# Kernel optimization log

Measured on AMD Instinct MI355X. Metric: run time of the kernel, lower is better.

The kernel has to match this reference:

```python
import jax, jax.numpy as jnp
import numpy as np

B = 4096      # batch
F = 16        # num fields
V = 20000     # field vocab size
E = 64        # embed size
HID = 1024    # hidden width (all hidden layers equal, required by the reshape trick)
NODE_IN = F * E  # 1024
NL = 3        # number of hidden layers stacked into attention (len(layer_sizes)-2)


def _xavier(key, shape):
    fan_in, fan_out = shape[0], shape[1]
    lim = np.sqrt(6.0 / (fan_in + fan_out)).astype(np.float32)
    return jax.random.uniform(key, shape, jnp.float32, -lim, lim)


def setup_inputs() -> dict:
    key = jax.random.key(0)
    ks = jax.random.split(key, 8)
    idx = jax.random.randint(ks[0], (B, F), 0, V)
    emb = _xavier(ks[1], (V, E))  # share init shape, then tile per-field via fold_in
    emb = jnp.stack([_xavier(jax.random.fold_in(ks[1], f), (V, E)) for f in range(F)], axis=0)  # [F,V,E]
    w0 = _xavier(ks[2], (NODE_IN, HID)); b0 = jnp.zeros((HID,), jnp.float32)
    w1 = _xavier(ks[3], (HID, HID));     b1 = jnp.zeros((HID,), jnp.float32)
    w2 = _xavier(ks[4], (HID, HID));     b2 = jnp.zeros((HID,), jnp.float32)
    w3 = _xavier(ks[5], (HID, HID));     b3 = jnp.zeros((HID,), jnp.float32)
    w_final = _xavier(ks[6], (2 * HID, 1)); b_final = jnp.zeros((1,), jnp.float32)
    return {"idx": idx, "emb": emb, "w0": w0, "b0": b0, "w1": w1, "b1": b1,
            "w2": w2, "b2": b2, "w3": w3, "b3": b3,
            "w_final": w_final, "b_final": b_final}


def reference(idx, emb, w0, b0, w1, b1, w2, b2, w3, b3, w_final, b_final):
    bsz = idx.shape[0]
    # sparse one-hot @ embed == gather: [B,F,E] -> [B, F*E]
    xw = emb[jnp.arange(F)[None, :], idx].reshape(bsz, F * E)
    # MLP stack (dropout in test mode: keep_prob=1, i.e. identity)
    l0 = jax.nn.relu(xw @ w0 + b0)
    l1 = jax.nn.relu(l0 @ w1 + b1)
    l2 = jax.nn.relu(l1 @ w2 + b2)
    l_final = jax.nn.relu(l2 @ w3 + b3)
    # faithful reproduction of tf.concat(axis=0) then reshape([-1, NL, HID])
    cat = jnp.concatenate([l0, l1, l2], axis=0)          # [NL*B, HID]
    Hm = cat.reshape(bsz, NL, HID)                        # H[b,j] = cat[NL*b + j]
    mask = 1.0 - jnp.eye(NL, dtype=Hm.dtype)              # zero diagonal
    S = jnp.einsum('bih,bjh->bij', Hm, Hm) * mask         # [B, NL, NL]
    A = jax.nn.softmax(S, axis=-1)                        # attention over layers
    G = jnp.einsum('bij,bjh->bh', A, Hm)                  # reduce_sum(A@H, axis=1)
    M = jnp.concatenate([l_final, G], axis=1)             # [B, 2*HID]
    out = (M @ w_final + b_final).squeeze(-1)             # logits [B]
    return out
```

## Files before the change

### kernel.cpp

```cpp
#include <hip/hip_runtime.h>
#include <hip/hip_bf16.h>
#include <stdint.h>

#define B_SZ 4096
#define F_N 16
#define V_SZ 20000
#define E_SZ 64
#define HID 1024

typedef __attribute__((ext_vector_type(8))) _Float16 f16x8;
typedef __attribute__((ext_vector_type(4))) _Float16 f16x4;
typedef __attribute__((ext_vector_type(4))) float f32x4;

__device__ __forceinline__ void gload16(const void* g, void* l) {
  __builtin_amdgcn_global_load_lds(
      (const __attribute__((address_space(1))) void*)g,
      (__attribute__((address_space(3))) void*)l, 16, 0, 0);
}

__device__ __forceinline__ int s3(int r) { return (r ^ (r >> 3)) & 7; }

__global__ __launch_bounds__(256) void prep(
    const int* __restrict__ idx, const float* __restrict__ emb,
    const float* __restrict__ w0, _Float16* __restrict__ wt0,
    _Float16* __restrict__ xw) {
  const int cb = blockIdx.x;
  const int t = threadIdx.x;
  if (cb < 512) {
    __shared__ float tile[64][33];
    const int k0 = (cb >> 5) * 64, n0 = (cb & 31) * 32;
    const int c = t & 31;
#pragma unroll
    for (int q = 0; q < 8; ++q) {
      int r = (t >> 5) + q * 8;
      tile[r][c] = w0[(size_t)(k0 + r) * HID + n0 + c];
    }
    __syncthreads();
#pragma unroll
    for (int q = 0; q < 4; ++q) {
      int s = t + q * 256;
      int n = s >> 5, c2 = s & 31;
      union { _Float16 h[2]; uint32_t u; } p;
      p.h[0] = (_Float16)tile[2 * c2][n];
      p.h[1] = (_Float16)tile[2 * c2 + 1][n];
      *(uint32_t*)(wt0 + (size_t)(n0 + n) * HID + k0 + 2 * c2) = p.u;
    }
  } else {
    int i = (cb - 512) * 256 + t;
    int b = i >> 8;
    int r = i & 255;
    int f = r >> 4;
    int e4 = r & 15;
    int id = idx[b * F_N + f];
    float4 v = *(const float4*)(emb + ((size_t)f * V_SZ + id) * E_SZ + e4 * 4);
    f16x4 h = {(_Float16)v.x, (_Float16)v.y, (_Float16)v.z, (_Float16)v.w};
    *(f16x4*)(xw + (size_t)b * HID + r * 4) = h;
  }
}

__global__ __launch_bounds__(512) void gemm_mfma(
    const _Float16* __restrict__ A, const _Float16* __restrict__ Wt,
    const float* __restrict__ bias, _Float16* __restrict__ C,
    const float* __restrict__ wnx, _Float16* __restrict__ wtnx) {
  __shared__ __align__(16) char shraw[65536];
  const int t = threadIdx.x;

  if (blockIdx.x >= 256) {
    const int cv = blockIdx.x - 256;
    float (*tile)[65] = (float(*)[65])shraw;
    const int k0 = (cv >> 4) * 64, n0 = (cv & 15) * 64;
    const int c = t & 63;
#pragma unroll
    for (int q = 0; q < 8; ++q) {
      int r = (t >> 6) + q * 8;
      tile[r][c] = wnx[(size_t)(k0 + r) * HID + n0 + c];
    }
    __syncthreads();
    {
      int n = t >> 3, ch = t & 7;
      f16x8 v;
#pragma unroll
      for (int j = 0; j < 8; ++j) v[j] = (_Float16)tile[ch * 8 + j][n];
      *(f16x8*)(wtnx + (size_t)(n0 + n) * HID + k0 + ch * 8) = v;
    }
    return;
  }

#define AS(b) ((_Float16*)(shraw + (b) * 32768))
#define BS(b) ((_Float16*)(shraw + (b) * 32768 + 16384))

  const int l = ((blockIdx.x & 7) << 5) | (blockIdx.x >> 3);
  const int bm = (l >> 3) * 128, bn = (l & 7) * 128;

  const int w = t >> 6, lane = t & 63;
  const int wk = w & 1, wn = (w >> 1) & 1, wm = w >> 2;
  const int lr = lane & 15, lg = lane >> 4;

  const int srow = t >> 3, cdst = t & 7;
  const int csrc = cdst ^ s3(srow);
  const _Float16* ga0 = A + (size_t)(bm + srow) * HID + csrc * 8;
  const _Float16* gb0 = Wt + (size_t)(bn + srow) * HID + csrc * 8;
  const int ld0 = t * 8, ld1 = t * 8 + 4096;

  int aoff[4], boff[4];
#pragma unroll
  for (int i = 0; i < 4; i++) {
    int ra = wm * 64 + i * 16 + lr;
    aoff[i] = ra * 64 + (((wk * 4 + lg) ^ s3(ra)) * 8);
    int rb = wn * 64 + i * 16 + lr;
    boff[i] = rb * 64 + (((wk * 4 + lg) ^ s3(rb)) * 8);
  }

  f32x4 acc[4][4] = {};

#define STAGE(buf, ko)                                   \
  gload16(ga0 + (ko), &AS(buf)[ld0]);                    \
  gload16(ga0 + (ko) + (size_t)64 * HID, &AS(buf)[ld1]); \
  gload16(gb0 + (ko), &BS(buf)[ld0]);                    \
  gload16(gb0 + (ko) + (size_t)64 * HID, &BS(buf)[ld1]);

  STAGE(0, 0)

  for (int tI = 0; tI < 16; ++tI) {
    const int cur = tI & 1;
    if (tI < 15) {
      STAGE(cur ^ 1, (tI + 1) * 64)
    }
    if (tI < 15)
      asm volatile("s_waitcnt vmcnt(4)" ::: "memory");
    else
      asm volatile("s_waitcnt vmcnt(0)" ::: "memory");
    asm volatile("s_barrier" ::: "memory");

    f16x8 a[4], b[4];
#pragma unroll
    for (int mi = 0; mi < 4; mi++) a[mi] = *(const f16x8*)&AS(cur)[aoff[mi]];
#pragma unroll
    for (int ni = 0; ni < 4; ni++) b[ni] = *(const f16x8*)&BS(cur)[boff[ni]];
#pragma unroll
    for (int mi = 0; mi < 4; mi++)
#pragma unroll
      for (int ni = 0; ni < 4; ni++)
        acc[mi][ni] = __builtin_amdgcn_mfma_f32_16x16x32_f16(
            b[ni], a[mi], acc[mi][ni], 0, 0, 0);

    asm volatile("s_barrier" ::: "memory");
  }
#undef STAGE

  float* red = (float*)shraw;
  float* R = red + ((wm << 1) | wn) * 4096;
  if (wk == 1) {
#pragma unroll
    for (int mi = 0; mi < 4; mi++)
#pragma unroll
      for (int ni = 0; ni < 4; ni++) {
        int u = mi * 16 + lr;
        int vb = ni * 4 + lg;
        *(f32x4*)&R[u * 64 + ((vb ^ lr) << 2)] = acc[mi][ni];
      }
  }
  asm volatile("s_barrier" ::: "memory");
  if (wk == 0) {
#pragma unroll
    for (int mi = 0; mi < 4; mi++)
#pragma unroll
      for (int ni = 0; ni < 4; ni++) {
        int u = mi * 16 + lr;
        int vb = ni * 4 + lg;
        f32x4 p = *(const f32x4*)&R[u * 64 + ((vb ^ lr) << 2)];
        acc[mi][ni] += p;
      }
#pragma unroll
    for (int ni = 0; ni < 4; ni++) {
      int colb = bn + wn * 64 + ni * 16 + lg * 4;
      float4 bv = *(const float4*)&bias[colb];
#pragma unroll
      for (int mi = 0; mi < 4; mi++) {
        int row = bm + wm * 64 + mi * 16 + lr;
        f16x4 hv;
        float x0 = acc[mi][ni][0] + bv.x;
        float x1 = acc[mi][ni][1] + bv.y;
        float x2 = acc[mi][ni][2] + bv.z;
        float x3 = acc[mi][ni][3] + bv.w;
        hv[0] = (_Float16)(x0 > 0.f ? x0 : 0.f);
        hv[1] = (_Float16)(x1 > 0.f ? x1 : 0.f);
        hv[2] = (_Float16)(x2 > 0.f ? x2 : 0.f);
        hv[3] = (_Float16)(x3 > 0.f ? x3 : 0.f);
        *(f16x4*)&C[(size_t)row * HID + colb] = hv;
      }
    }
  }
#undef AS
#undef BS
}

__global__ __launch_bounds__(256) void attn_final(
    const _Float16* __restrict__ cat, const _Float16* __restrict__ lf,
    const float* __restrict__ wf, const float* __restrict__ bfin,
    float* __restrict__ out) {
  const int wave = threadIdx.x >> 6;
  const int lane = threadIdx.x & 63;
  const int b = blockIdx.x * 4 + wave;

  const _Float16* h0 = cat + (size_t)(3 * b + 0) * 1024;
  const _Float16* h1 = cat + (size_t)(3 * b + 1) * 1024;
  const _Float16* h2 = cat + (size_t)(3 * b + 2) * 1024;
  const _Float16* lfr = lf + (size_t)b * 1024;

  float s01 = 0.f, s02 = 0.f, s12 = 0.f;
  float d0 = 0.f, d1 = 0.f, d2 = 0.f, dl = 0.f;

#pragma unroll
  for (int q = 0; q < 2; ++q) {
    int e8 = (lane + q * 64) * 8;
    f16x8 a0 = *(const f16x8*)(h0 + e8);
    f16x8 a1 = *(const f16x8*)(h1 + e8);
    f16x8 a2 = *(const f16x8*)(h2 + e8);
    f16x8 al = *(const f16x8*)(lfr + e8);
    float4 u0a = *(const float4*)(wf + e8);
    float4 u0b = *(const float4*)(wf + e8 + 4);
    float4 u1a = *(const float4*)(wf + 1024 + e8);
    float4 u1b = *(const float4*)(wf + 1024 + e8 + 4);
    float wf0[8] = {u0a.x, u0a.y, u0a.z, u0a.w, u0b.x, u0b.y, u0b.z, u0b.w};
    float wf1[8] = {u1a.x, u1a.y, u1a.z, u1a.w, u1b.x, u1b.y, u1b.z, u1b.w};
#pragma unroll
    for (int j = 0; j < 8; ++j) {
      float p0 = (float)a0[j], p1 = (float)a1[j], p2 = (float)a2[j];
      float pl = (float)al[j];
      s01 = fmaf(p0, p1, s01);
      s02 = fmaf(p0, p2, s02);
      s12 = fmaf(p1, p2, s12);
      d0 = fmaf(p0, wf1[j], d0);
      d1 = fmaf(p1, wf1[j], d1);
      d2 = fmaf(p2, wf1[j], d2);
      dl = fmaf(pl, wf0[j], dl);
    }
  }

#pragma unroll
  for (int m = 1; m < 64; m <<= 1) {
    s01 += __shfl_xor(s01, m);
    s02 += __shfl_xor(s02, m);
    s12 += __shfl_xor(s12, m);
    d0 += __shfl_xor(d0, m);
    d1 += __shfl_xor(d1, m);
    d2 += __shfl_xor(d2, m);
    dl += __shfl_xor(dl, m);
  }

  if (lane == 0) {
    float c0 = 0.f, c1 = 0.f, c2 = 0.f;
    {
      float m = fmaxf(0.f, fmaxf(s01, s02));
      float e0 = expf(0.f - m), e1 = expf(s01 - m), e2 = expf(s02 - m);
      float inv = 1.f / (e0 + e1 + e2);
      c0 += e0 * inv; c1 += e1 * inv; c2 += e2 * inv;
    }
    {
      float m = fmaxf(s01, fmaxf(0.f, s12));
      float e0 = expf(s01 - m), e1 = expf(0.f - m), e2 = expf(s12 - m);
      float inv = 1.f / (e0 + e1 + e2);
      c0 += e0 * inv; c1 += e1 * inv; c2 += e2 * inv;
    }
    {
      float m = fmaxf(s02, fmaxf(s12, 0.f));
      float e0 = expf(s02 - m), e1 = expf(s12 - m), e2 = expf(0.f - m);
      float inv = 1.f / (e0 + e1 + e2);
      c0 += e0 * inv; c1 += e1 * inv; c2 += e2 * inv;
    }
    out[b] = dl + c0 * d0 + c1 * d1 + c2 * d2 + bfin[0];
  }
}

extern "C" void kernel_launch(void* const* d_in, const int* in_sizes, int n_in,
                              void* d_out, int out_size, void* d_ws,
                              size_t ws_size, hipStream_t stream) {
  const int* idx = (const int*)d_in[0];
  const float* emb = (const float*)d_in[1];
  const float* w0 = (const float*)d_in[2];
  const float* b0 = (const float*)d_in[3];
  const float* w1 = (const float*)d_in[4];
  const float* b1 = (const float*)d_in[5];
  const float* w2 = (const float*)d_in[6];
  const float* b2 = (const float*)d_in[7];
  const float* w3 = (const float*)d_in[8];
  const float* b3 = (const float*)d_in[9];
  const float* wf = (const float*)d_in[10];
  const float* bfin = (const float*)d_in[11];
  float* out = (float*)d_out;

  const size_t RB = (size_t)B_SZ * HID;
  const size_t WSZ = (size_t)HID * HID;

  _Float16* wt = (_Float16*)d_ws;
  _Float16* xw16 = wt + 4 * WSZ;
  _Float16* cat16 = xw16 + RB;
  _Float16* lf16 = cat16 + 3 * RB;

  prep<<<4608, 256, 0, stream>>>(idx, emb, w0, wt, xw16);

  gemm_mfma<<<512, 512, 0, stream>>>(xw16, wt + 0 * WSZ, b0, cat16,
                                     w1, wt + 1 * WSZ);
  gemm_mfma<<<512, 512, 0, stream>>>(cat16, wt + 1 * WSZ, b1, cat16 + RB,
                                     w2, wt + 2 * WSZ);
  gemm_mfma<<<512, 512, 0, stream>>>(cat16 + RB, wt + 2 * WSZ, b2,
                                     cat16 + 2 * RB, w3, wt + 3 * WSZ);
  gemm_mfma<<<256, 512, 0, stream>>>(cat16 + 2 * RB, wt + 3 * WSZ, b3, lf16,
                                     (const float*)nullptr,
                                     (_Float16*)nullptr);

  attn_final<<<B_SZ / 4, 256, 0, stream>>>(cat16, lf16, wf, bfin, out);
}
```

Baseline: 76.73 us.

## Fuse four MLP GEMMs into one persistent kernel with per-panel flags

Moves all four weight transposes into the prep kernel and replaces the four separate GEMM launches with a single persistent 256-block kernel. Each block loops over the layers and waits on an atomic counter for its 128-row panel of the previous layer before starting the next. This removes the launch gaps and the full-grid drain between layers, letting layers overlap across panels. The risks are spin-wait stalls and a deadlock if all 256 blocks cannot be resident at once.

```diff
diff --git a/kernel.cpp b/kernel.cpp
--- a/kernel.cpp
+++ b/kernel.cpp
@@ -22,18 +22,23 @@
 
 __global__ __launch_bounds__(256) void prep(
     const int* __restrict__ idx, const float* __restrict__ emb,
-    const float* __restrict__ w0, _Float16* __restrict__ wt0,
-    _Float16* __restrict__ xw) {
+    const float* __restrict__ w0, const float* __restrict__ w1,
+    const float* __restrict__ w2, const float* __restrict__ w3,
+    _Float16* __restrict__ wt, _Float16* __restrict__ xw,
+    int* __restrict__ flags) {
   const int cb = blockIdx.x;
   const int t = threadIdx.x;
-  if (cb < 512) {
+  if (cb < 2048) {
+    const int z = cb >> 9, rem = cb & 511;
+    const float* w = (z == 0) ? w0 : (z == 1) ? w1 : (z == 2) ? w2 : w3;
+    _Float16* outp = wt + (size_t)z * HID * HID;
     __shared__ float tile[64][33];
-    const int k0 = (cb >> 5) * 64, n0 = (cb & 31) * 32;
+    const int k0 = (rem >> 5) * 64, n0 = (rem & 31) * 32;
     const int c = t & 31;
 #pragma unroll
     for (int q = 0; q < 8; ++q) {
       int r = (t >> 5) + q * 8;
-      tile[r][c] = w0[(size_t)(k0 + r) * HID + n0 + c];
+      tile[r][c] = w[(size_t)(k0 + r) * HID + n0 + c];
     }
     __syncthreads();
 #pragma unroll
@@ -43,10 +48,11 @@
       union { _Float16 h[2]; uint32_t u; } p;
       p.h[0] = (_Float16)tile[2 * c2][n];
       p.h[1] = (_Float16)tile[2 * c2 + 1][n];
-      *(uint32_t*)(wt0 + (size_t)(n0 + n) * HID + k0 + 2 * c2) = p.u;
+      *(uint32_t*)(outp + (size_t)(n0 + n) * HID + k0 + 2 * c2) = p.u;
     }
   } else {
-    int i = (cb - 512) * 256 + t;
+    if (cb == 2048 && t < 96) flags[t] = 0;
+    int i = (cb - 2048) * 256 + t;
     int b = i >> 8;
     int r = i & 255;
     int f = r >> 4;
@@ -58,48 +64,30 @@
   }
 }
 
-__global__ __launch_bounds__(512) void gemm_mfma(
-    const _Float16* __restrict__ A, const _Float16* __restrict__ Wt,
-    const float* __restrict__ bias, _Float16* __restrict__ C,
-    const float* __restrict__ wnx, _Float16* __restrict__ wtnx) {
+__global__ __launch_bounds__(512) void gemm4_fused(
+    const _Float16* __restrict__ xw, const _Float16* __restrict__ wt,
+    const float* __restrict__ b0, const float* __restrict__ b1,
+    const float* __restrict__ b2, const float* __restrict__ b3,
+    _Float16* __restrict__ cat, _Float16* __restrict__ lf,
+    int* __restrict__ flags) {
   __shared__ __align__(16) char shraw[65536];
-  const int t = threadIdx.x;
-
-  if (blockIdx.x >= 256) {
-    const int cv = blockIdx.x - 256;
-    float (*tile)[65] = (float(*)[65])shraw;
-    const int k0 = (cv >> 4) * 64, n0 = (cv & 15) * 64;
-    const int c = t & 63;
-#pragma unroll
-    for (int q = 0; q < 8; ++q) {
-      int r = (t >> 6) + q * 8;
-      tile[r][c] = wnx[(size_t)(k0 + r) * HID + n0 + c];
-    }
-    __syncthreads();
-    {
-      int n = t >> 3, ch = t & 7;
-      f16x8 v;
-#pragma unroll
-      for (int j = 0; j < 8; ++j) v[j] = (_Float16)tile[ch * 8 + j][n];
-      *(f16x8*)(wtnx + (size_t)(n0 + n) * HID + k0 + ch * 8) = v;
-    }
-    return;
-  }
-
 #define AS(b) ((_Float16*)(shraw + (b) * 32768))
 #define BS(b) ((_Float16*)(shraw + (b) * 32768 + 16384))
 
+  const int t = threadIdx.x;
   const int l = ((blockIdx.x & 7) << 5) | (blockIdx.x >> 3);
   const int bm = (l >> 3) * 128, bn = (l & 7) * 128;
+  const int panel = l >> 3;
 
   const int w = t >> 6, lane = t & 63;
   const int wk = w & 1, wn = (w >> 1) & 1, wm = w >> 2;
   const int lr = lane & 15, lg = lane >> 4;
 
+  const size_t RB = (size_t)B_SZ * HID;
+  const size_t WSZ = (size_t)HID * HID;
+
   const int srow = t >> 3, cdst = t & 7;
   const int csrc = cdst ^ s3(srow);
-  const _Float16* ga0 = A + (size_t)(bm + srow) * HID + csrc * 8;
-  const _Float16* gb0 = Wt + (size_t)(bn + srow) * HID + csrc * 8;
   const int ld0 = t * 8, ld1 = t * 8 + 4096;
 
   int aoff[4], boff[4];
@@ -111,86 +99,113 @@
     boff[i] = rb * 64 + (((wk * 4 + lg) ^ s3(rb)) * 8);
   }
 
-  f32x4 acc[4][4] = {};
-
 #define STAGE(buf, ko)                                   \
   gload16(ga0 + (ko), &AS(buf)[ld0]);                    \
   gload16(ga0 + (ko) + (size_t)64 * HID, &AS(buf)[ld1]); \
   gload16(gb0 + (ko), &BS(buf)[ld0]);                    \
   gload16(gb0 + (ko) + (size_t)64 * HID, &BS(buf)[ld1]);
 
-  STAGE(0, 0)
-
-  for (int tI = 0; tI < 16; ++tI) {
-    const int cur = tI & 1;
-    if (tI < 15) {
-      STAGE(cur ^ 1, (tI + 1) * 64)
-    }
-    if (tI < 15)
-      asm volatile("s_waitcnt vmcnt(4)" ::: "memory");
-    else
-      asm volatile("s_waitcnt vmcnt(0)" ::: "memory");
+  for (int L = 0; L < 4; ++L) {
+    const _Float16* A = (L == 0) ? xw : cat + (size_t)(L - 1) * RB;
+    _Float16* C = (L == 3) ? lf : cat + (size_t)L * RB;
+    const float* bias = (L == 0) ? b0 : (L == 1) ? b1 : (L == 2) ? b2 : b3;
+    const _Float16* Wt = wt + (size_t)L * WSZ;
+
+    if (L > 0) {
+      if (t == 0) {
+        while (__hip_atomic_load(&flags[(L - 1) * 32 + panel],
+                                 __ATOMIC_ACQUIRE,
+                                 __HIP_MEMORY_SCOPE_AGENT) < 8)
+          __builtin_amdgcn_s_sleep(2);
+      }
+      __syncthreads();
+    }
+
+    const _Float16* ga0 = A + (size_t)(bm + srow) * HID + csrc * 8;
+    const _Float16* gb0 = Wt + (size_t)(bn + srow) * HID + csrc * 8;
+
+    f32x4 acc[4][4] = {};
+
+    STAGE(0, 0)
+
+    for (int tI = 0; tI < 16; ++tI) {
+      const int cur = tI & 1;
+      if (tI < 15) {
+        STAGE(cur ^ 1, (tI + 1) * 64)
+      }
+      if (tI < 15)
+        asm volatile("s_waitcnt vmcnt(4)" ::: "memory");
+      else
+        asm volatile("s_waitcnt vmcnt(0)" ::: "memory");
+      asm volatile("s_barrier" ::: "memory");
+
+      f16x8 a[4], b[4];
+#pragma unroll
+      for (int mi = 0; mi < 4; mi++) a[mi] = *(const f16x8*)&AS(cur)[aoff[mi]];
+#pragma unroll
+      for (int ni = 0; ni < 4; ni++) b[ni] = *(const f16x8*)&BS(cur)[boff[ni]];
+#pragma unroll
+      for (int mi = 0; mi < 4; mi++)
+#pragma unroll
+        for (int ni = 0; ni < 4; ni++)
+          acc[mi][ni] = __builtin_amdgcn_mfma_f32_16x16x32_f16(
+              b[ni], a[mi], acc[mi][ni], 0, 0, 0);
+
+      asm volatile("s_barrier" ::: "memory");
+    }
+
+    float* red = (float*)shraw;
+    float* R = red + ((wm << 1) | wn) * 4096;
+    if (wk == 1) {
+#pragma unroll
+      for (int mi = 0; mi < 4; mi++)
+#pragma unroll
+        for (int ni = 0; ni < 4; ni++) {
+          int u = mi * 16 + lr;
+          int vb = ni * 4 + lg;
+          *(f32x4*)&R[u * 64 + ((vb ^ lr) << 2)] = acc[mi][ni];
+        }
+    }
     asm volatile("s_barrier" ::: "memory");
-
-    f16x8 a[4], b[4];
-#pragma unroll
-    for (int mi = 0; mi < 4; mi++) a[mi] = *(const f16x8*)&AS(cur)[aoff[mi]];
-#pragma unroll
-    for (int ni = 0; ni < 4; ni++) b[ni] = *(const f16x8*)&BS(cur)[boff[ni]];
-#pragma unroll
-    for (int mi = 0; mi < 4; mi++)
-#pragma unroll
-      for (int ni = 0; ni < 4; ni++)
-        acc[mi][ni] = __builtin_amdgcn_mfma_f32_16x16x32_f16(
-            b[ni], a[mi], acc[mi][ni], 0, 0, 0);
-
-    asm volatile("s_barrier" ::: "memory");
+    if (wk == 0) {
+#pragma unroll
+      for (int mi = 0; mi < 4; mi++)
+#pragma unroll
+        for (int ni = 0; ni < 4; ni++) {
+          int u = mi * 16 + lr;
+          int vb = ni * 4 + lg;
+          f32x4 p = *(const f32x4*)&R[u * 64 + ((vb ^ lr) << 2)];
+          acc[mi][ni] += p;
+        }
+#pragma unroll
+      for (int ni = 0; ni < 4; ni++) {
+        int colb = bn + wn * 64 + ni * 16 + lg * 4;
+        float4 bv = *(const float4*)&bias[colb];
+#pragma unroll
+        for (int mi = 0; mi < 4; mi++) {
+          int row = bm + wm * 64 + mi * 16 + lr;
+          f16x4 hv;
+          float x0 = acc[mi][ni][0] + bv.x;
+          float x1 = acc[mi][ni][1] + bv.y;
+          float x2 = acc[mi][ni][2] + bv.z;
+          float x3 = acc[mi][ni][3] + bv.w;
+          hv[0] = (_Float16)(x0 > 0.f ? x0 : 0.f);
+          hv[1] = (_Float16)(x1 > 0.f ? x1 : 0.f);
+          hv[2] = (_Float16)(x2 > 0.f ? x2 : 0.f);
+          hv[3] = (_Float16)(x3 > 0.f ? x3 : 0.f);
+          *(f16x4*)&C[(size_t)row * HID + colb] = hv;
+        }
+      }
+    }
+
+    __syncthreads();
+    if (L < 3 && t == 0) {
+      __threadfence();
+      __hip_atomic_fetch_add(&flags[L * 32 + panel], 1, __ATOMIC_RELEASE,
+                             __HIP_MEMORY_SCOPE_AGENT);
+    }
   }
 #undef STAGE
-
-  float* red = (float*)shraw;
-  float* R = red + ((wm << 1) | wn) * 4096;
-  if (wk == 1) {
-#pragma unroll
-    for (int mi = 0; mi < 4; mi++)
-#pragma unroll
-      for (int ni = 0; ni < 4; ni++) {
-        int u = mi * 16 + lr;
-        int vb = ni * 4 + lg;
-        *(f32x4*)&R[u * 64 + ((vb ^ lr) << 2)] = acc[mi][ni];
-      }
-  }
-  asm volatile("s_barrier" ::: "memory");
-  if (wk == 0) {
-#pragma unroll
-    for (int mi = 0; mi < 4; mi++)
-#pragma unroll
-      for (int ni = 0; ni < 4; ni++) {
-        int u = mi * 16 + lr;
-        int vb = ni * 4 + lg;
-        f32x4 p = *(const f32x4*)&R[u * 64 + ((vb ^ lr) << 2)];
-        acc[mi][ni] += p;
-      }
-#pragma unroll
-    for (int ni = 0; ni < 4; ni++) {
-      int colb = bn + wn * 64 + ni * 16 + lg * 4;
-      float4 bv = *(const float4*)&bias[colb];
-#pragma unroll
-      for (int mi = 0; mi < 4; mi++) {
-        int row = bm + wm * 64 + mi * 16 + lr;
-        f16x4 hv;
-        float x0 = acc[mi][ni][0] + bv.x;
-        float x1 = acc[mi][ni][1] + bv.y;
-        float x2 = acc[mi][ni][2] + bv.z;
-        float x3 = acc[mi][ni][3] + bv.w;
-        hv[0] = (_Float16)(x0 > 0.f ? x0 : 0.f);
-        hv[1] = (_Float16)(x1 > 0.f ? x1 : 0.f);
-        hv[2] = (_Float16)(x2 > 0.f ? x2 : 0.f);
-        hv[3] = (_Float16)(x3 > 0.f ? x3 : 0.f);
-        *(f16x4*)&C[(size_t)row * HID + colb] = hv;
-      }
-    }
-  }
 #undef AS
 #undef BS
 }
@@ -297,18 +312,12 @@
   _Float16* xw16 = wt + 4 * WSZ;
   _Float16* cat16 = xw16 + RB;
   _Float16* lf16 = cat16 + 3 * RB;
-
-  prep<<<4608, 256, 0, stream>>>(idx, emb, w0, wt, xw16);
-
-  gemm_mfma<<<512, 512, 0, stream>>>(xw16, wt + 0 * WSZ, b0, cat16,
-                                     w1, wt + 1 * WSZ);
-  gemm_mfma<<<512, 512, 0, stream>>>(cat16, wt + 1 * WSZ, b1, cat16 + RB,
-                                     w2, wt + 2 * WSZ);
-  gemm_mfma<<<512, 512, 0, stream>>>(cat16 + RB, wt + 2 * WSZ, b2,
-                                     cat16 + 2 * RB, w3, wt + 3 * WSZ);
-  gemm_mfma<<<256, 512, 0, stream>>>(cat16 + 2 * RB, wt + 3 * WSZ, b3, lf16,
-                                     (const float*)nullptr,
-                                     (_Float16*)nullptr);
+  int* flags = (int*)(lf16 + RB);
+
+  prep<<<6144, 256, 0, stream>>>(idx, emb, w0, w1, w2, w3, wt, xw16, flags);
+
+  gemm4_fused<<<256, 512, 0, stream>>>(xw16, wt, b0, b1, b2, b3, cat16, lf16,
+                                       flags);
 
   attn_final<<<B_SZ / 4, 256, 0, stream>>>(cat16, lf16, wf, bfin, out);
 }
```

Result: slower. 115.4 us (+50.3%).
